# Performance work log

Measured on AMD Instinct MI355X. Metric: run time of the kernel, lower is better.

Reference implementation:

```python
import jax, jax.numpy as jnp
import numpy as np

N_NODES = 50000
N_EDGES = 800000
IN_FEATS = 256
HIDDEN = 256
NUM_CLASSES = 64


def setup_inputs() -> dict:
    key = jax.random.key(0)
    k1, k2, k3, k4 = jax.random.split(key, 4)
    features = jax.random.normal(k1, (N_NODES, IN_FEATS), dtype=jnp.float32)
    edge_index = jax.random.randint(k2, (2, N_EDGES), 0, N_NODES, dtype=jnp.int32)
    W1 = jax.random.normal(k3, (IN_FEATS, HIDDEN), dtype=jnp.float32) * (1.0 / np.sqrt(IN_FEATS))
    b1 = jnp.zeros((HIDDEN,), dtype=jnp.float32)
    W2 = jax.random.normal(k4, (HIDDEN, NUM_CLASSES), dtype=jnp.float32) * (1.0 / np.sqrt(HIDDEN))
    b2 = jnp.zeros((NUM_CLASSES,), dtype=jnp.float32)
    return {"features": features, "edge_index": edge_index, "W1": W1, "b1": b1, "W2": W2, "b2": b2}


def reference(features, edge_index, W1, b1, W2, b2):
    # Two-layer GCN: h = A_hat @ relu(A_hat @ X W1 + b1) W2 + b2
    # A_hat uses symmetric degree normalization 1/sqrt(d_src * d_dst)
    N = features.shape[0]
    src, dst = edge_index[0], edge_index[1]
    ones = jnp.ones((src.shape[0],), dtype=features.dtype)
    deg_out = jax.ops.segment_sum(ones, src, num_segments=N)  # out-degree per node
    deg_in = jax.ops.segment_sum(ones, dst, num_segments=N)   # in-degree per node
    inv_sqrt_out = jax.lax.rsqrt(jnp.maximum(deg_out, 1.0))
    inv_sqrt_in = jax.lax.rsqrt(jnp.maximum(deg_in, 1.0))
    edge_norm = (inv_sqrt_out[src] * inv_sqrt_in[dst])[:, None]  # [E,1]

    def gcn_layer(x, W, b):
        h = x @ W                      # transform first (reduces message width)
        msg = h[src] * edge_norm       # [E, out]
        agg = jax.ops.segment_sum(msg, dst, num_segments=N)
        return agg + b

    h = jax.nn.relu(gcn_layer(features, W1, b1))
    return gcn_layer(h, W2, b2)
```

## Files before the change

kernel.cpp:

```cpp
#include <hip/hip_runtime.h>

#define NN 50000
#define MPAD 50048
#define NE 800000
#define SCAN_BLOCKS 49

typedef short short8 __attribute__((ext_vector_type(8)));
typedef float f32x4 __attribute__((ext_vector_type(4)));

__device__ __forceinline__ unsigned short f2bf(float x) {
    unsigned u = __builtin_bit_cast(unsigned, x);
    u += 0x7FFFu + ((u >> 16) & 1u);
    return (unsigned short)(u >> 16);
}
__device__ __forceinline__ float bf2f(unsigned short h) {
    unsigned u = ((unsigned)h) << 16;
    return __builtin_bit_cast(float, u);
}
__device__ __forceinline__ void gld16(const void* g, void* l) {
    __builtin_amdgcn_global_load_lds(
        (const __attribute__((address_space(1))) unsigned int*)g,
        (__attribute__((address_space(3))) unsigned int*)l, 16, 0, 0);
}
__device__ __forceinline__ void nt_store8(void* p, ushort4 v) {
    __builtin_nontemporal_store(__builtin_bit_cast(unsigned long long, v),
                                (unsigned long long*)p);
}


__global__ __launch_bounds__(256) void count_kernel(const int* __restrict__ src,
    const int* __restrict__ dst, int* __restrict__ cnt_out, int* __restrict__ cnt_in, int E)
{
    int e = blockIdx.x * 256 + threadIdx.x;
    if (e < E) {
        atomicAdd(&cnt_out[src[e]], 1);
        atomicAdd(&cnt_in[dst[e]], 1);
    }
}

__global__ __launch_bounds__(256) void scanA_kernel(const int* __restrict__ cnt,
    int* __restrict__ bsum)
{
    __shared__ int sm[256];
    int b = blockIdx.x, tid = threadIdx.x;
    int base = b * 1024 + tid * 4;
    int s = 0;
    #pragma unroll
    for (int i = 0; i < 4; ++i) {
        int idx = base + i;
        if (idx < NN) s += cnt[idx];
    }
    sm[tid] = s;
    __syncthreads();
    for (int off = 128; off > 0; off >>= 1) {
        if (tid < off) sm[tid] += sm[tid + off];
        __syncthreads();
    }
    if (tid == 0) bsum[b] = sm[0];
}

__global__ __launch_bounds__(64) void scanB_kernel(const int* __restrict__ bsum,
    int* __restrict__ bexcl)
{
    int tid = threadIdx.x;
    int orig = (tid < SCAN_BLOCKS) ? bsum[tid] : 0;
    int v = orig;
    #pragma unroll
    for (int off = 1; off < 64; off <<= 1) {
        int u = __shfl_up(v, off, 64);
        if (tid >= off) v += u;
    }
    if (tid < SCAN_BLOCKS) bexcl[tid] = v - orig;
}

__global__ __launch_bounds__(256) void scanC_kernel(const int* __restrict__ cnt,
    const int* __restrict__ cnt_out, const int* __restrict__ bexcl,
    int* __restrict__ rs, float* __restrict__ inv_out, float* __restrict__ inv_in)
{
    __shared__ int wsum[4];
    int b = blockIdx.x, tid = threadIdx.x;
    int lane = tid & 63, wv = tid >> 6;
    int base = b * 1024 + tid * 4;
    int v[4]; int s = 0;
    #pragma unroll
    for (int i = 0; i < 4; ++i) {
        int idx = base + i;
        v[i] = (idx < NN) ? cnt[idx] : 0;
        s += v[i];
    }
    int inc = s;
    #pragma unroll
    for (int off = 1; off < 64; off <<= 1) {
        int u = __shfl_up(inc, off, 64);
        if (lane >= off) inc += u;
    }
    if (lane == 63) wsum[wv] = inc;
    __syncthreads();
    int wo = 0;
    for (int i = 0; i < wv; ++i) wo += wsum[i];
    int run = wo + (inc - s) + bexcl[b];
    #pragma unroll
    for (int i = 0; i < 4; ++i) {
        int idx = base + i;
        if (idx < NN) {
            rs[idx] = run; run += v[i];
            inv_in[idx]  = rsqrtf(fmaxf((float)v[i], 1.0f));
            inv_out[idx] = rsqrtf(fmaxf((float)cnt_out[idx], 1.0f));
        }
    }
}

__global__ __launch_bounds__(256) void fill_kernel(const int* __restrict__ src,
    const int* __restrict__ dst, int* __restrict__ rs, int* __restrict__ csr_src, int E)
{
    int e = blockIdx.x * 256 + threadIdx.x;
    if (e < E) {
        int slot = atomicAdd(&rs[dst[e]], 1);
        csr_src[slot] = src[e];
    }
}

__global__ __launch_bounds__(256) void splitW_kernel(const float* __restrict__ W1,
    const float* __restrict__ W2, unsigned short* __restrict__ W1T,
    unsigned short* __restrict__ W2T)
{
    int i = blockIdx.x * 256 + threadIdx.x;
    const float* W; unsigned short* BT; int N; int ii;
    if (i < 256 * 32) { W = W1; BT = W1T; N = 256; ii = i; }
    else if (i < 256 * 32 + 64 * 32) { W = W2; BT = W2T; N = 64; ii = i - 256 * 32; }
    else return;
    int col = ii >> 5, kc = ii & 31;
    short8 hv, lv;
    #pragma unroll
    for (int j = 0; j < 8; ++j) {
        float x = W[(size_t)(kc * 8 + j) * N + col];
        unsigned short h = f2bf(x);
        hv[j] = (short)h;
        lv[j] = (short)f2bf(x - bf2f(h));
    }
    size_t base = (size_t)col * 512;
    size_t o = (kc >> 3) * 64 + (((kc & 7) ^ (col & 7)) * 8);
    *(short8*)&BT[base + o] = hv;
    *(short8*)&BT[base + 256 + o] = lv;
}

__global__ __launch_bounds__(256) void gemm1_fuse_kernel(const float* __restrict__ X,
    const unsigned short* __restrict__ BT, const float* __restrict__ inv_out,
    unsigned short* __restrict__ C, int M)
{
    constexpr int BN = 128, WN = 64, NF = 4;
    __shared__ unsigned short Ash[128 * 64];
    __shared__ unsigned short Asl[128 * 64];
    __shared__ unsigned short Bsh[BN * 64];
    __shared__ unsigned short Bsl[BN * 64];
    const int tid = threadIdx.x;
    const int w = tid >> 6, lane = tid & 63;
    const int wm = w >> 1, wn = w & 1;
    const int r = lane & 15, kg = lane >> 4;
    const int rowbase = blockIdx.x * 128;
    const int colbase = blockIdx.y * BN;

    f32x4 acc[4][NF] = {};

    for (int kb = 0; kb < 4; ++kb) {
        #pragma unroll
        for (int i = 0; i < 4; ++i) {
            int ct = (w * 4 + i) * 64 + lane;
            int row = ct >> 3, c = ct & 7;
            int grow = rowbase + row; if (grow >= NN) grow = NN - 1;
            const float* sp = X + (size_t)grow * 256 + kb * 64 + c * 8;
            float4 x0 = *(const float4*)sp;
            float4 x1 = *(const float4*)(sp + 4);
            float xs[8] = {x0.x, x0.y, x0.z, x0.w, x1.x, x1.y, x1.z, x1.w};
            short8 hv, lv;
            #pragma unroll
            for (int t = 0; t < 8; ++t) {
                unsigned short h = f2bf(xs[t]);
                hv[t] = (short)h;
                lv[t] = (short)f2bf(xs[t] - bf2f(h));
            }
            int dsto = row * 64 + ((c ^ (row & 7)) * 8);
            *(short8*)&Ash[dsto] = hv;
            *(short8*)&Asl[dsto] = lv;
        }
        #pragma unroll
        for (int i = 0; i < 4; ++i) {
            int ct = (w * 4 + i) * 64 + lane;
            int col = ct >> 3, c = ct & 7;
            size_t goff = (size_t)(colbase + col) * 512 + kb * 64 + c * 8;
            gld16(BT + goff, (unsigned short*)Bsh + (size_t)ct * 8);
            gld16(BT + goff + 256, (unsigned short*)Bsl + (size_t)ct * 8);
        }
        __syncthreads();
        #pragma unroll
        for (int ks = 0; ks < 2; ++ks) {
            short8 ahf[4], alf[4];
            #pragma unroll
            for (int mf = 0; mf < 4; ++mf) {
                int row = wm * 64 + mf * 16 + r;
                int lo = row * 64 + (((ks * 4 + kg) ^ (row & 7)) * 8);
                ahf[mf] = *(const short8*)&Ash[lo];
                alf[mf] = *(const short8*)&Asl[lo];
            }
            #pragma unroll
            for (int nf = 0; nf < NF; ++nf) {
                int col = wn * WN + nf * 16 + r;
                int lo = col * 64 + (((ks * 4 + kg) ^ (col & 7)) * 8);
                short8 bh = *(const short8*)&Bsh[lo];
                short8 bl = *(const short8*)&Bsl[lo];
                #pragma unroll
                for (int mf = 0; mf < 4; ++mf) {
                    acc[mf][nf] = __builtin_amdgcn_mfma_f32_16x16x32_bf16(ahf[mf], bh, acc[mf][nf], 0, 0, 0);
                    acc[mf][nf] = __builtin_amdgcn_mfma_f32_16x16x32_bf16(alf[mf], bh, acc[mf][nf], 0, 0, 0);
                    acc[mf][nf] = __builtin_amdgcn_mfma_f32_16x16x32_bf16(ahf[mf], bl, acc[mf][nf], 0, 0, 0);
                }
            }
        }
        __syncthreads();
    }

    #pragma unroll
    for (int mf = 0; mf < 4; ++mf) {
        #pragma unroll
        for (int reg = 0; reg < 4; ++reg) {
            int orow = rowbase + wm * 64 + mf * 16 + kg * 4 + reg;
            if (orow >= M) continue;
            float sc = inv_out[orow];
            #pragma unroll
            for (int nf = 0; nf < NF; ++nf) {
                int ocol = colbase + wn * WN + nf * 16 + r;
                C[(size_t)orow * 256 + ocol] = f2bf(acc[mf][nf][reg] * sc);
            }
        }
    }
}

__global__ __launch_bounds__(256) void gemm2_kernel(
    const unsigned short* __restrict__ Ah, const unsigned short* __restrict__ Al,
    const unsigned short* __restrict__ BT, const float* __restrict__ inv_out,
    unsigned short* __restrict__ C, int M)
{
    constexpr int BN = 64, WN = 32, NF = 2, BI = 2;
    __shared__ unsigned short Ash[128 * 64];
    __shared__ unsigned short Asl[128 * 64];
    __shared__ unsigned short Bsh[BN * 64];
    __shared__ unsigned short Bsl[BN * 64];
    const int tid = threadIdx.x;
    const int w = tid >> 6, lane = tid & 63;
    const int wm = w >> 1, wn = w & 1;
    const int r = lane & 15, kg = lane >> 4;
    const int rowbase = blockIdx.x * 128;

    f32x4 acc[4][NF] = {};

    for (int kb = 0; kb < 4; ++kb) {
        #pragma unroll
        for (int i = 0; i < 4; ++i) {
            int ct = (w * 4 + i) * 64 + lane;
            int row = ct >> 3, c = ct & 7;
            size_t goff = (size_t)(rowbase + row) * 256 + kb * 64 + c * 8;
            gld16(Ah + goff, (unsigned short*)Ash + (size_t)ct * 8);
            gld16(Al + goff, (unsigned short*)Asl + (size_t)ct * 8);
        }
        #pragma unroll
        for (int i = 0; i < BI; ++i) {
            int ct = (w * BI + i) * 64 + lane;
            int col = ct >> 3, c = ct & 7;
            size_t goff = (size_t)col * 512 + kb * 64 + c * 8;
            gld16(BT + goff, (unsigned short*)Bsh + (size_t)ct * 8);
            gld16(BT + goff + 256, (unsigned short*)Bsl + (size_t)ct * 8);
        }
        __syncthreads();
        #pragma unroll
        for (int ks = 0; ks < 2; ++ks) {
            short8 ahf[4], alf[4];
            #pragma unroll
            for (int mf = 0; mf < 4; ++mf) {
                int row = wm * 64 + mf * 16 + r;
                int lo = row * 64 + (((ks * 4 + kg) ^ (row & 7)) * 8);
                ahf[mf] = *(const short8*)&Ash[lo];
                alf[mf] = *(const short8*)&Asl[lo];
            }
            #pragma unroll
            for (int nf = 0; nf < NF; ++nf) {
                int col = wn * WN + nf * 16 + r;
                int lo = col * 64 + (((ks * 4 + kg) ^ (col & 7)) * 8);
                short8 bh = *(const short8*)&Bsh[lo];
                short8 bl = *(const short8*)&Bsl[lo];
                #pragma unroll
                for (int mf = 0; mf < 4; ++mf) {
                    acc[mf][nf] = __builtin_amdgcn_mfma_f32_16x16x32_bf16(ahf[mf], bh, acc[mf][nf], 0, 0, 0);
                    acc[mf][nf] = __builtin_amdgcn_mfma_f32_16x16x32_bf16(alf[mf], bh, acc[mf][nf], 0, 0, 0);
                    acc[mf][nf] = __builtin_amdgcn_mfma_f32_16x16x32_bf16(ahf[mf], bl, acc[mf][nf], 0, 0, 0);
                }
            }
        }
        __syncthreads();
    }

    #pragma unroll
    for (int mf = 0; mf < 4; ++mf) {
        #pragma unroll
        for (int reg = 0; reg < 4; ++reg) {
            int orow = rowbase + wm * 64 + mf * 16 + kg * 4 + reg;
            if (orow >= M) continue;
            float sc = inv_out[orow];
            #pragma unroll
            for (int nf = 0; nf < NF; ++nf) {
                int ocol = wn * WN + nf * 16 + r;
                C[(size_t)orow * 64 + ocol] = f2bf(acc[mf][nf][reg] * sc);
            }
        }
    }
}

__global__ __launch_bounds__(256) void gather256_kernel(const unsigned short* __restrict__ t1,
    const int* __restrict__ csr_src, const int* __restrict__ rs,
    const float* __restrict__ inv_in, const float* __restrict__ b1,
    unsigned short* __restrict__ Ah2, unsigned short* __restrict__ Al2)
{
    int n = (int)((blockIdx.x * 256 + threadIdx.x) >> 6);
    int lane = threadIdx.x & 63;
    if (n >= NN) return;
    int begin = (n == 0) ? 0 : rs[n - 1];
    int end = rs[n];
    float a0 = 0.f, a1 = 0.f, a2 = 0.f, a3 = 0.f;
    int j = begin;
    for (; j + 8 <= end; j += 8) {
        int s0 = csr_src[j],     s1 = csr_src[j + 1], s2 = csr_src[j + 2], s3 = csr_src[j + 3];
        int s4 = csr_src[j + 4], s5 = csr_src[j + 5], s6 = csr_src[j + 6], s7 = csr_src[j + 7];
        ushort4 v0 = *(const ushort4*)&t1[(size_t)s0 * 256 + lane * 4];
        ushort4 v1 = *(const ushort4*)&t1[(size_t)s1 * 256 + lane * 4];
        ushort4 v2 = *(const ushort4*)&t1[(size_t)s2 * 256 + lane * 4];
        ushort4 v3 = *(const ushort4*)&t1[(size_t)s3 * 256 + lane * 4];
        ushort4 v4 = *(const ushort4*)&t1[(size_t)s4 * 256 + lane * 4];
        ushort4 v5 = *(const ushort4*)&t1[(size_t)s5 * 256 + lane * 4];
        ushort4 v6 = *(const ushort4*)&t1[(size_t)s6 * 256 + lane * 4];
        ushort4 v7 = *(const ushort4*)&t1[(size_t)s7 * 256 + lane * 4];
        a0 += bf2f(v0.x); a1 += bf2f(v0.y); a2 += bf2f(v0.z); a3 += bf2f(v0.w);
        a0 += bf2f(v1.x); a1 += bf2f(v1.y); a2 += bf2f(v1.z); a3 += bf2f(v1.w);
        a0 += bf2f(v2.x); a1 += bf2f(v2.y); a2 += bf2f(v2.z); a3 += bf2f(v2.w);
        a0 += bf2f(v3.x); a1 += bf2f(v3.y); a2 += bf2f(v3.z); a3 += bf2f(v3.w);
        a0 += bf2f(v4.x); a1 += bf2f(v4.y); a2 += bf2f(v4.z); a3 += bf2f(v4.w);
        a0 += bf2f(v5.x); a1 += bf2f(v5.y); a2 += bf2f(v5.z); a3 += bf2f(v5.w);
        a0 += bf2f(v6.x); a1 += bf2f(v6.y); a2 += bf2f(v6.z); a3 += bf2f(v6.w);
        a0 += bf2f(v7.x); a1 += bf2f(v7.y); a2 += bf2f(v7.z); a3 += bf2f(v7.w);
    }
    for (; j < end; ++j) {
        int s = csr_src[j];
        ushort4 v = *(const ushort4*)&t1[(size_t)s * 256 + lane * 4];
        a0 += bf2f(v.x); a1 += bf2f(v.y); a2 += bf2f(v.z); a3 += bf2f(v.w);
    }
    float win = inv_in[n];
    int f0 = lane * 4;
    float4 bb = *(const float4*)&b1[f0];
    float x0 = fmaxf(fmaf(a0, win, bb.x), 0.f);
    float x1 = fmaxf(fmaf(a1, win, bb.y), 0.f);
    float x2 = fmaxf(fmaf(a2, win, bb.z), 0.f);
    float x3 = fmaxf(fmaf(a3, win, bb.w), 0.f);
    unsigned short h0 = f2bf(x0), h1 = f2bf(x1), h2 = f2bf(x2), h3 = f2bf(x3);
    ushort4 hv = {h0, h1, h2, h3};
    ushort4 lv = {f2bf(x0 - bf2f(h0)), f2bf(x1 - bf2f(h1)),
                  f2bf(x2 - bf2f(h2)), f2bf(x3 - bf2f(h3))};
    int kb = f0 >> 6, c = (f0 >> 3) & 7, e = f0 & 7;
    size_t off = (size_t)n * 256 + kb * 64 + ((c ^ (n & 7)) * 8) + e;
    nt_store8(&Ah2[off], hv);
    nt_store8(&Al2[off], lv);
}

__global__ __launch_bounds__(256) void gather64_kernel(const unsigned short* __restrict__ t2,
    const int* __restrict__ csr_src, const int* __restrict__ rs,
    const float* __restrict__ inv_in, const float* __restrict__ b2,
    float* __restrict__ out)
{
    int n = (int)((blockIdx.x * 256 + threadIdx.x) >> 6);
    int lane = threadIdx.x & 63;
    if (n >= NN) return;
    int begin = (n == 0) ? 0 : rs[n - 1];
    int end = rs[n];
    float acc = 0.f;
    int j = begin;
    for (; j + 8 <= end; j += 8) {
        int s0 = csr_src[j],     s1 = csr_src[j + 1], s2 = csr_src[j + 2], s3 = csr_src[j + 3];
        int s4 = csr_src[j + 4], s5 = csr_src[j + 5], s6 = csr_src[j + 6], s7 = csr_src[j + 7];
        float v0 = bf2f(t2[(size_t)s0 * 64 + lane]);
        float v1 = bf2f(t2[(size_t)s1 * 64 + lane]);
        float v2 = bf2f(t2[(size_t)s2 * 64 + lane]);
        float v3 = bf2f(t2[(size_t)s3 * 64 + lane]);
        float v4 = bf2f(t2[(size_t)s4 * 64 + lane]);
        float v5 = bf2f(t2[(size_t)s5 * 64 + lane]);
        float v6 = bf2f(t2[(size_t)s6 * 64 + lane]);
        float v7 = bf2f(t2[(size_t)s7 * 64 + lane]);
        acc += v0; acc += v1; acc += v2; acc += v3;
        acc += v4; acc += v5; acc += v6; acc += v7;
    }
    for (; j < end; ++j) {
        int s = csr_src[j];
        acc += bf2f(t2[(size_t)s * 64 + lane]);
    }
    float o = fmaf(acc, inv_in[n], b2[lane]);
    __builtin_nontemporal_store(o, &out[(size_t)n * 64 + lane]);
}

extern "C" void kernel_launch(void* const* d_in, const int* in_sizes, int n_in,
                              void* d_out, int out_size, void* d_ws, size_t ws_size,
                              hipStream_t stream)
{
    const float* features = (const float*)d_in[0];
    const int*   edge_index = (const int*)d_in[1];
    const float* W1 = (const float*)d_in[2];
    const float* b1 = (const float*)d_in[3];
    const float* W2 = (const float*)d_in[4];
    const float* b2 = (const float*)d_in[5];
    float* out = (float*)d_out;
    const int* src = edge_index;
    const int* dst = edge_index + NE;

    char* p = (char*)d_ws;
    int* cnt_out = (int*)p;            p += (size_t)NN * 4;
    int* cnt_in  = (int*)p;            p += (size_t)NN * 4;
    float* inv_out = (float*)p;        p += (size_t)NN * 4;
    float* inv_in  = (float*)p;        p += (size_t)NN * 4;
    int* rs      = (int*)p;            p += (size_t)NN * 4;
    int* csr_src = (int*)p;            p += (size_t)NE * 4;
    int* bsum    = (int*)p;            p += 64 * 4;
    int* bexcl   = (int*)p;            p += 64 * 4;
    unsigned short* W1T = (unsigned short*)p;  p += (size_t)256 * 512 * 2;
    unsigned short* W2T = (unsigned short*)p;  p += (size_t)64 * 512 * 2;
    unsigned short* t1  = (unsigned short*)p;  p += (size_t)NN * 256 * 2;
    unsigned short* Ah2 = (unsigned short*)p;  p += (size_t)MPAD * 256 * 2;
    unsigned short* Al2 = (unsigned short*)p;  p += (size_t)MPAD * 256 * 2;
    unsigned short* t2  = (unsigned short*)p;  p += (size_t)NN * 64 * 2;

    hipMemsetAsync(cnt_out, 0, 2 * (size_t)NN * sizeof(int), stream);

    count_kernel<<<(NE + 255) / 256, 256, 0, stream>>>(src, dst, cnt_out, cnt_in, NE);
    scanA_kernel<<<SCAN_BLOCKS, 256, 0, stream>>>(cnt_in, bsum);
    scanB_kernel<<<1, 64, 0, stream>>>(bsum, bexcl);
    scanC_kernel<<<SCAN_BLOCKS, 256, 0, stream>>>(cnt_in, cnt_out, bexcl, rs, inv_out, inv_in);
    fill_kernel<<<(NE + 255) / 256, 256, 0, stream>>>(src, dst, rs, csr_src, NE);

    splitW_kernel<<<(320 * 32 + 255) / 256, 256, 0, stream>>>(W1, W2, W1T, W2T);

    gemm1_fuse_kernel<<<dim3(MPAD / 128, 2), 256, 0, stream>>>(
        features, W1T, inv_out, t1, NN);

    gather256_kernel<<<(NN * 64 + 255) / 256, 256, 0, stream>>>(
        t1, csr_src, rs, inv_in, b1, Ah2, Al2);

    gemm2_kernel<<<MPAD / 128, 256, 0, stream>>>(
        Ah2, Al2, W2T, inv_out, t2, NN);

    gather64_kernel<<<(NN * 64 + 255) / 256, 256, 0, stream>>>(
        t2, csr_src, rs, inv_in, b2, out);
}
```

Measured before the change: 300.6 us.

## Fuse CSR build, degree scan and weight split into one cooperative kernel

Replaces the memset plus six small preprocessing launches (count, three scan phases, fill, weight split) with a single cooperative kernel that uses grid-wide syncs between phases. The goal is to remove per-launch overhead and the idle gaps between tiny dependent kernels. In exchange the grid is capped at 1024 resident blocks, so the edge loops become grid-stride loops, and each grid.sync has its own cost. The scan phases now run on only 49 of those blocks while the rest wait.

Result: slower. 773.2 us (+157.2%).

```diff
diff --git a/kernel.cpp b/kernel.cpp
--- a/kernel.cpp
+++ b/kernel.cpp
@@ -1,9 +1,13 @@
 #include <hip/hip_runtime.h>
+#include <hip/hip_cooperative_groups.h>
+
+namespace cg = cooperative_groups;
 
 #define NN 50000
 #define MPAD 50048
 #define NE 800000
 #define SCAN_BLOCKS 49
+#define COOP_BLOCKS 1024
 
 typedef short short8 __attribute__((ext_vector_type(8)));
 typedef float f32x4 __attribute__((ext_vector_type(4)));
@@ -27,121 +31,116 @@
                                 (unsigned long long*)p);
 }
 
-
-__global__ __launch_bounds__(256) void count_kernel(const int* __restrict__ src,
-    const int* __restrict__ dst, int* __restrict__ cnt_out, int* __restrict__ cnt_in, int E)
-{
-    int e = blockIdx.x * 256 + threadIdx.x;
-    if (e < E) {
+__global__ __launch_bounds__(256) void csr_build_kernel(
+    const int* __restrict__ src, const int* __restrict__ dst,
+    const float* __restrict__ W1, const float* __restrict__ W2,
+    unsigned short* __restrict__ W1T, unsigned short* __restrict__ W2T,
+    int* __restrict__ cnt_out, int* __restrict__ cnt_in,
+    int* __restrict__ bsum, int* __restrict__ bexcl, int* __restrict__ rs,
+    float* __restrict__ inv_out, float* __restrict__ inv_in,
+    int* __restrict__ csr_src)
+{
+    cg::grid_group grid = cg::this_grid();
+    __shared__ int sm[256];
+    const int tid = threadIdx.x;
+    const int gtid = blockIdx.x * 256 + tid;
+    const int gsz = COOP_BLOCKS * 256;
+
+    for (int i = gtid; i < 2 * NN; i += gsz) cnt_out[i] = 0;
+    for (int i = gtid; i < 320 * 32; i += gsz) {
+        const float* W; unsigned short* BT; int N; int ii;
+        if (i < 256 * 32) { W = W1; BT = W1T; N = 256; ii = i; }
+        else { W = W2; BT = W2T; N = 64; ii = i - 256 * 32; }
+        int col = ii >> 5, kc = ii & 31;
+        short8 hv, lv;
+        #pragma unroll
+        for (int j = 0; j < 8; ++j) {
+            float x = W[(size_t)(kc * 8 + j) * N + col];
+            unsigned short h = f2bf(x);
+            hv[j] = (short)h;
+            lv[j] = (short)f2bf(x - bf2f(h));
+        }
+        size_t base = (size_t)col * 512;
+        size_t o = (kc >> 3) * 64 + (((kc & 7) ^ (col & 7)) * 8);
+        *(short8*)&BT[base + o] = hv;
+        *(short8*)&BT[base + 256 + o] = lv;
+    }
+    grid.sync();
+
+    for (int e = gtid; e < NE; e += gsz) {
         atomicAdd(&cnt_out[src[e]], 1);
         atomicAdd(&cnt_in[dst[e]], 1);
     }
-}
-
-__global__ __launch_bounds__(256) void scanA_kernel(const int* __restrict__ cnt,
-    int* __restrict__ bsum)
-{
-    __shared__ int sm[256];
-    int b = blockIdx.x, tid = threadIdx.x;
-    int base = b * 1024 + tid * 4;
-    int s = 0;
-    #pragma unroll
-    for (int i = 0; i < 4; ++i) {
-        int idx = base + i;
-        if (idx < NN) s += cnt[idx];
-    }
-    sm[tid] = s;
-    __syncthreads();
-    for (int off = 128; off > 0; off >>= 1) {
-        if (tid < off) sm[tid] += sm[tid + off];
-        __syncthreads();
-    }
-    if (tid == 0) bsum[b] = sm[0];
-}
-
-__global__ __launch_bounds__(64) void scanB_kernel(const int* __restrict__ bsum,
-    int* __restrict__ bexcl)
-{
-    int tid = threadIdx.x;
-    int orig = (tid < SCAN_BLOCKS) ? bsum[tid] : 0;
-    int v = orig;
-    #pragma unroll
-    for (int off = 1; off < 64; off <<= 1) {
-        int u = __shfl_up(v, off, 64);
-        if (tid >= off) v += u;
-    }
-    if (tid < SCAN_BLOCKS) bexcl[tid] = v - orig;
-}
-
-__global__ __launch_bounds__(256) void scanC_kernel(const int* __restrict__ cnt,
-    const int* __restrict__ cnt_out, const int* __restrict__ bexcl,
-    int* __restrict__ rs, float* __restrict__ inv_out, float* __restrict__ inv_in)
-{
-    __shared__ int wsum[4];
-    int b = blockIdx.x, tid = threadIdx.x;
-    int lane = tid & 63, wv = tid >> 6;
-    int base = b * 1024 + tid * 4;
-    int v[4]; int s = 0;
-    #pragma unroll
-    for (int i = 0; i < 4; ++i) {
-        int idx = base + i;
-        v[i] = (idx < NN) ? cnt[idx] : 0;
-        s += v[i];
-    }
-    int inc = s;
-    #pragma unroll
-    for (int off = 1; off < 64; off <<= 1) {
-        int u = __shfl_up(inc, off, 64);
-        if (lane >= off) inc += u;
-    }
-    if (lane == 63) wsum[wv] = inc;
-    __syncthreads();
-    int wo = 0;
-    for (int i = 0; i < wv; ++i) wo += wsum[i];
-    int run = wo + (inc - s) + bexcl[b];
-    #pragma unroll
-    for (int i = 0; i < 4; ++i) {
-        int idx = base + i;
-        if (idx < NN) {
-            rs[idx] = run; run += v[i];
-            inv_in[idx]  = rsqrtf(fmaxf((float)v[i], 1.0f));
-            inv_out[idx] = rsqrtf(fmaxf((float)cnt_out[idx], 1.0f));
-        }
-    }
-}
-
-__global__ __launch_bounds__(256) void fill_kernel(const int* __restrict__ src,
-    const int* __restrict__ dst, int* __restrict__ rs, int* __restrict__ csr_src, int E)
-{
-    int e = blockIdx.x * 256 + threadIdx.x;
-    if (e < E) {
+    grid.sync();
+
+    if (blockIdx.x < SCAN_BLOCKS) {
+        int base = blockIdx.x * 1024 + tid * 4;
+        int s = 0;
+        #pragma unroll
+        for (int i = 0; i < 4; ++i) {
+            int idx = base + i;
+            if (idx < NN) s += cnt_in[idx];
+        }
+        sm[tid] = s;
+        __syncthreads();
+        for (int off = 128; off > 0; off >>= 1) {
+            if (tid < off) sm[tid] += sm[tid + off];
+            __syncthreads();
+        }
+        if (tid == 0) bsum[blockIdx.x] = sm[0];
+    }
+    grid.sync();
+
+    if (blockIdx.x == 0 && tid < 64) {
+        int orig = (tid < SCAN_BLOCKS) ? bsum[tid] : 0;
+        int v = orig;
+        #pragma unroll
+        for (int off = 1; off < 64; off <<= 1) {
+            int u = __shfl_up(v, off, 64);
+            if (tid >= off) v += u;
+        }
+        if (tid < SCAN_BLOCKS) bexcl[tid] = v - orig;
+    }
+    grid.sync();
+
+    if (blockIdx.x < SCAN_BLOCKS) {
+        int lane = tid & 63, wv = tid >> 6;
+        int base = blockIdx.x * 1024 + tid * 4;
+        int v[4]; int s = 0;
+        #pragma unroll
+        for (int i = 0; i < 4; ++i) {
+            int idx = base + i;
+            v[i] = (idx < NN) ? cnt_in[idx] : 0;
+            s += v[i];
+        }
+        int inc = s;
+        #pragma unroll
+        for (int off = 1; off < 64; off <<= 1) {
+            int u = __shfl_up(inc, off, 64);
+            if (lane >= off) inc += u;
+        }
+        __syncthreads();
+        if (lane == 63) sm[wv] = inc;
+        __syncthreads();
+        int wo = 0;
+        for (int i = 0; i < wv; ++i) wo += sm[i];
+        int run = wo + (inc - s) + bexcl[blockIdx.x];
+        #pragma unroll
+        for (int i = 0; i < 4; ++i) {
+            int idx = base + i;
+            if (idx < NN) {
+                rs[idx] = run; run += v[i];
+                inv_in[idx]  = rsqrtf(fmaxf((float)v[i], 1.0f));
+                inv_out[idx] = rsqrtf(fmaxf((float)cnt_out[idx], 1.0f));
+            }
+        }
+    }
+    grid.sync();
+
+    for (int e = gtid; e < NE; e += gsz) {
         int slot = atomicAdd(&rs[dst[e]], 1);
         csr_src[slot] = src[e];
     }
-}
-
-__global__ __launch_bounds__(256) void splitW_kernel(const float* __restrict__ W1,
-    const float* __restrict__ W2, unsigned short* __restrict__ W1T,
-    unsigned short* __restrict__ W2T)
-{
-    int i = blockIdx.x * 256 + threadIdx.x;
-    const float* W; unsigned short* BT; int N; int ii;
-    if (i < 256 * 32) { W = W1; BT = W1T; N = 256; ii = i; }
-    else if (i < 256 * 32 + 64 * 32) { W = W2; BT = W2T; N = 64; ii = i - 256 * 32; }
-    else return;
-    int col = ii >> 5, kc = ii & 31;
-    short8 hv, lv;
-    #pragma unroll
-    for (int j = 0; j < 8; ++j) {
-        float x = W[(size_t)(kc * 8 + j) * N + col];
-        unsigned short h = f2bf(x);
-        hv[j] = (short)h;
-        lv[j] = (short)f2bf(x - bf2f(h));
-    }
-    size_t base = (size_t)col * 512;
-    size_t o = (kc >> 3) * 64 + (((kc & 7) ^ (col & 7)) * 8);
-    *(short8*)&BT[base + o] = hv;
-    *(short8*)&BT[base + 256 + o] = lv;
 }
 
 __global__ __launch_bounds__(256) void gemm1_fuse_kernel(const float* __restrict__ X,
@@ -432,15 +431,14 @@
     unsigned short* Al2 = (unsigned short*)p;  p += (size_t)MPAD * 256 * 2;
     unsigned short* t2  = (unsigned short*)p;  p += (size_t)NN * 64 * 2;
 
-    hipMemsetAsync(cnt_out, 0, 2 * (size_t)NN * sizeof(int), stream);
-
-    count_kernel<<<(NE + 255) / 256, 256, 0, stream>>>(src, dst, cnt_out, cnt_in, NE);
-    scanA_kernel<<<SCAN_BLOCKS, 256, 0, stream>>>(cnt_in, bsum);
-    scanB_kernel<<<1, 64, 0, stream>>>(bsum, bexcl);
-    scanC_kernel<<<SCAN_BLOCKS, 256, 0, stream>>>(cnt_in, cnt_out, bexcl, rs, inv_out, inv_in);
-    fill_kernel<<<(NE + 255) / 256, 256, 0, stream>>>(src, dst, rs, csr_src, NE);
-
-    splitW_kernel<<<(320 * 32 + 255) / 256, 256, 0, stream>>>(W1, W2, W1T, W2T);
+    void* cargs[] = {
+        (void*)&src, (void*)&dst, (void*)&W1, (void*)&W2,
+        (void*)&W1T, (void*)&W2T, (void*)&cnt_out, (void*)&cnt_in,
+        (void*)&bsum, (void*)&bexcl, (void*)&rs,
+        (void*)&inv_out, (void*)&inv_in, (void*)&csr_src
+    };
+    hipLaunchCooperativeKernel((void*)csr_build_kernel, dim3(COOP_BLOCKS), dim3(256),
+                               cargs, 0, stream);
 
     gemm1_fuse_kernel<<<dim3(MPAD / 128, 2), 256, 0, stream>>>(
         features, W1T, inv_out, t1, NN);
```
